# Kernel tuning notes

Hardware: AMD Instinct MI355X
Metric: run time of the kernel (lower is better)

The kernel has to match this reference:

```python
import jax, jax.numpy as jnp
import numpy as np

LEVEL_SHAPES = ((128, 128), (64, 64), (32, 32), (16, 16))  # (H_l, W_l) per level
B, LQ, C, H, L, P, DFF = 4, 1024, 256, 8, 4, 4, 1024
DH = C // H
LSRC = sum(h * w for h, w in LEVEL_SHAPES)
NORMALIZER = np.array([[w, h] for h, w in LEVEL_SHAPES], dtype=np.float32)  # (L,2) as (W,H)


def layer_norm(x, g, b, eps=1e-5):
    m = jnp.mean(x, -1, keepdims=True)
    v = jnp.var(x, -1, keepdims=True)
    return (x - m) * jax.lax.rsqrt(v + eps) * g + b


def mha(tgt, query_pos, w_in, b_in, w_out, b_out):
    # nn.MultiheadAttention with q=k=tgt+pos, v=tgt (eval mode, no dropout)
    qk = tgt + query_pos
    q = (qk @ w_in[:C].T + b_in[:C]).reshape(B, LQ, H, DH)
    k = (qk @ w_in[C:2 * C].T + b_in[C:2 * C]).reshape(B, LQ, H, DH)
    v = (tgt @ w_in[2 * C:].T + b_in[2 * C:]).reshape(B, LQ, H, DH)
    att = jax.nn.softmax(jnp.einsum('bqhd,bkhd->bhqk', q, k) / np.float32(np.sqrt(DH)), axis=-1)
    o = jnp.einsum('bhqk,bkhd->bqhd', att, v).reshape(B, LQ, C)
    return o @ w_out.T + b_out


def ms_deform_attn(query, ref, src, off_w, off_b, aw_w, aw_b, val_w, val_b, out_w, out_b):
    value = (src @ val_w.T + val_b).reshape(B, LSRC, H, DH)
    offsets = (query @ off_w.T + off_b).reshape(B, LQ, H, L, P, 2)
    aw = jax.nn.softmax((query @ aw_w.T + aw_b).reshape(B, LQ, H, L * P), axis=-1)
    aw = aw.reshape(B, LQ, H, L, P)
    # sampling locations in [0,1], offsets normalized per level by (W_l, H_l)
    loc = ref[:, :, None, :, None, :] + offsets / NORMALIZER[None, None, None, :, None, :]
    out = jnp.zeros((B, LQ, H, DH), query.dtype)
    start = 0
    for l, (h, w) in enumerate(LEVEL_SHAPES):
        v = value[:, start:start + h * w].reshape(B, h, w, H, DH)
        v = v.transpose(0, 3, 1, 2, 4).reshape(B, H, h * w, DH)  # [B,H,hw,DH]
        start += h * w
        # grid_sample semantics: align_corners=False, zero padding
        x = loc[:, :, :, l, :, 0] * w - 0.5  # [B,LQ,H,P]
        y = loc[:, :, :, l, :, 1] * h - 0.5
        x0 = jnp.floor(x); y0 = jnp.floor(y)
        x0i = x0.astype(jnp.int32); y0i = y0.astype(jnp.int32)
        wx1 = x - x0; wx0 = 1.0 - wx1
        wy1 = y - y0; wy0 = 1.0 - wy1

        def gather(ix, iy):
            valid = ((ix >= 0) & (ix < w) & (iy >= 0) & (iy < h)).astype(v.dtype)
            idx = jnp.clip(iy, 0, h - 1) * w + jnp.clip(ix, 0, w - 1)
            idx = idx.transpose(0, 2, 1, 3).reshape(B, H, LQ * P)
            g = jnp.take_along_axis(v, idx[..., None], axis=2).reshape(B, H, LQ, P, DH)
            return g * valid.transpose(0, 2, 1, 3)[..., None]

        def wmul(ww):
            return ww.transpose(0, 2, 1, 3)[..., None]  # [B,H,LQ,P,1]

        s = (gather(x0i, y0i) * wmul(wx0 * wy0)
             + gather(x0i + 1, y0i) * wmul(wx1 * wy0)
             + gather(x0i, y0i + 1) * wmul(wx0 * wy1)
             + gather(x0i + 1, y0i + 1) * wmul(wx1 * wy1))
        out = out + jnp.einsum('bhqpd,bqhp->bqhd', s, aw[:, :, :, l])
    return out.reshape(B, LQ, C) @ out_w.T + out_b


def setup_inputs():
    key = jax.random.key(0)
    ks = jax.random.split(key, 16)

    def n(i, shape, s=0.02):
        return jax.random.normal(ks[i], shape, jnp.float32) * s

    z = lambda *s: jnp.zeros(s, jnp.float32)
    o = lambda *s: jnp.ones(s, jnp.float32)
    return {
        'tgt': n(0, (B, LQ, C), 1.0),
        'query_pos': n(1, (B, LQ, C), 1.0),
        'reference_points': jax.random.uniform(ks[2], (B, LQ, L, 2), jnp.float32),
        'src': n(3, (B, LSRC, C), 1.0),
        'in_w': n(4, (3 * C, C)), 'in_b': z(3 * C),
        'sa_w': n(5, (C, C)), 'sa_b': z(C),
        'off_w': n(6, (H * L * P * 2, C)), 'off_b': n(7, (H * L * P * 2,), 2.0),
        'aw_w': n(8, (H * L * P, C)), 'aw_b': z(H * L * P),
        'val_w': n(9, (C, C)), 'val_b': z(C),
        'co_w': n(10, (C, C)), 'co_b': z(C),
        'ln1_g': o(C), 'ln1_b': z(C),
        'ln2_g': o(C), 'ln2_b': z(C),
        'ln3_g': o(C), 'ln3_b': z(C),
        'f1_w': n(11, (DFF, C)), 'f1_b': z(DFF),
        'f2_w': n(12, (C, DFF)), 'f2_b': z(C),
    }


def reference(tgt, query_pos, reference_points, src, in_w, in_b, sa_w, sa_b,
              off_w, off_b, aw_w, aw_b, val_w, val_b, co_w, co_b,
              ln1_g, ln1_b, ln2_g, ln2_b, ln3_g, ln3_b,
              f1_w, f1_b, f2_w, f2_b):
    # self-attention + residual + norm2
    tgt2 = mha(tgt, query_pos, in_w, in_b, sa_w, sa_b)
    tgt = layer_norm(tgt + tgt2, ln2_g, ln2_b)
    # multi-scale deformable cross-attention + residual + norm1 (DETR path)
    tgt2 = ms_deform_attn(tgt + query_pos, reference_points, src,
                          off_w, off_b, aw_w, aw_b, val_w, val_b, co_w, co_b)
    tgt = layer_norm(tgt + tgt2, ln1_g, ln1_b)
    # FFN + residual + norm3
    tgt2 = jax.nn.relu(tgt @ f1_w.T + f1_b) @ f2_w.T + f2_b
    tgt = layer_norm(tgt + tgt2, ln3_g, ln3_b)
    return tgt
```

## Files before the change

### kernel.cpp

```cpp
#include <hip/hip_runtime.h>
#include <hip/hip_bf16.h>
#include <math.h>

#define Bv   4
#define LQv  1024
#define Cv   256
#define Hv   8
#define Lv   4
#define Pv   4
#define DFFv 1024
#define DHv  32
#define LSRCv 21760

typedef __attribute__((ext_vector_type(8))) short bhalf8;
typedef __attribute__((ext_vector_type(4))) float floatx4;

__device__ inline unsigned pk_bf16x2(float x, float y) {
    unsigned xb = __float_as_uint(x), yb = __float_as_uint(y);
    unsigned xr = (xb + 0x7FFFu + ((xb >> 16) & 1u)) >> 16;
    unsigned yr = (yb + 0x7FFFu + ((yb >> 16) & 1u)) >> 16;
    return xr | (yr << 16);
}
__device__ inline unsigned short bf16_1(float x) {
    unsigned xb = __float_as_uint(x);
    return (unsigned short)((xb + 0x7FFFu + ((xb >> 16) & 1u)) >> 16);
}
__device__ inline float ubf2f(unsigned short u) {
    return __uint_as_float(((unsigned)u) << 16);
}

__global__ __launch_bounds__(256) void cvt_weights(const float* __restrict__ in_w,
                                                   const float* __restrict__ sa_w,
                                                   const float* __restrict__ val_w,
                                                   const float* __restrict__ off_w,
                                                   const float* __restrict__ aw_w,
                                                   const float* __restrict__ co_w,
                                                   const float* __restrict__ f1_w,
                                                   const float* __restrict__ f2_w,
                                                   const float* __restrict__ off_b,
                                                   const float* __restrict__ aw_b,
                                                   unsigned short* __restrict__ wp,
                                                   float* __restrict__ cbias) {
    const size_t idx4 = (size_t)blockIdx.x * 256 + threadIdx.x;
    if (idx4 >= 253952) {
        const int t = (int)(idx4 - 253952);
        if (t < 256) cbias[t] = off_b[t];
        else if (t < 384) cbias[t] = aw_b[t - 256];
        return;
    }
    const size_t f = idx4 * 4;
    const float* src; size_t off; int K; size_t obase; int nadd = 0;
    if (f < 196608)      { src = in_w;  off = f;          K = 256;  obase = 0; }
    else if (f < 262144) { src = sa_w;  off = f - 196608; K = 256;  obase = 196608; }
    else if (f < 327680) { src = val_w; off = f - 262144; K = 256;  obase = 262144; }
    else if (f < 393216) { src = off_w; off = f - 327680; K = 256;  obase = 327680; }
    else if (f < 425984) { src = aw_w;  off = f - 393216; K = 256;  obase = 327680; nadd = 256; }
    else if (f < 491520) { src = co_w;  off = f - 425984; K = 256;  obase = 425984; }
    else if (f < 753664) { src = f1_w;  off = f - 491520; K = 256;  obase = 491520; }
    else                 { src = f2_w;  off = f - 753664; K = 1024; obase = 753664; }
    float4 v = *(const float4*)(src + off);
    const int n = (int)(off / (size_t)K) + nadd, k = (int)(off % (size_t)K);
    const size_t di = obase + ((size_t)((n >> 4) * (K >> 5) + (k >> 5))) * 512
                    + (size_t)(((k >> 3) & 3) * 128 + (n & 15) * 8 + (k & 7));
    *(uint2*)(wp + di) = (uint2){pk_bf16x2(v.x, v.y), pk_bf16x2(v.z, v.w)};
}

__global__ __launch_bounds__(256, 4) void gemm_mfma(const float* __restrict__ A,
                                                    const float* __restrict__ A2,
                                                    const unsigned short* __restrict__ Wp,
                                                    const float* __restrict__ bias,
                                                    float* __restrict__ Cf,
                                                    unsigned short* __restrict__ Ch,
                                                    int M, int N, int K, int relu) {
    __shared__ __attribute__((aligned(16))) unsigned short As[2][64 * 136];
    const unsigned bid = blockIdx.x;
    const unsigned nc = (unsigned)N >> 6;
    const unsigned xcd = bid & 7, j = bid >> 3;
    const unsigned cpan = j % nc, r8 = j / nc;
    const int bm = (int)((xcd + (r8 << 3)) << 6);
    const int bn = (int)(cpan << 6);
    const int tid = threadIdx.x;
    const int wid = tid >> 6, lane = tid & 63;
    const int wr = wid >> 1, wc = wid & 1;
    const int col16 = lane & 15;
    const int quad = lane >> 4;

    const int srow0 = tid >> 4;
    const int scol = (tid & 15) * 4;
    const float* asrc = A + (size_t)(bm + srow0) * K + scol;
    const float* a2src = A2 ? A2 + (size_t)(bm + srow0) * K + scol : nullptr;

    const int K32 = K >> 5;
    const unsigned short* wbase = Wp + ((size_t)((bn >> 4) + wc * 2) * K32) * 512
                                + (size_t)lane * 8;

    floatx4 acc[2][2] = {};
    float4 rv[4][2];

    auto loadA = [&](int c) {
#pragma unroll
        for (int j2 = 0; j2 < 4; ++j2)
#pragma unroll
            for (int i = 0; i < 2; ++i)
                rv[j2][i] = *(const float4*)(asrc + (size_t)(16 * j2) * K + c * 128 + 64 * i);
        if (a2src) {
#pragma unroll
            for (int j2 = 0; j2 < 4; ++j2)
#pragma unroll
                for (int i = 0; i < 2; ++i) {
                    float4 t = *(const float4*)(a2src + (size_t)(16 * j2) * K + c * 128 + 64 * i);
                    rv[j2][i].x += t.x; rv[j2][i].y += t.y;
                    rv[j2][i].z += t.z; rv[j2][i].w += t.w;
                }
        }
    };
    auto writeA = [&](int buf) {
#pragma unroll
        for (int j2 = 0; j2 < 4; ++j2)
#pragma unroll
            for (int i = 0; i < 2; ++i) {
                uint2 p = {pk_bf16x2(rv[j2][i].x, rv[j2][i].y),
                           pk_bf16x2(rv[j2][i].z, rv[j2][i].w)};
                *(uint2*)&As[buf][(srow0 + 16 * j2) * 136 + scol + 64 * i] = p;
            }
    };

    const int NC = K >> 7;
    loadA(0);
    writeA(0);

    for (int c = 0; c < NC; ++c) {
        __syncthreads();
        if (c + 1 < NC) loadA(c + 1);

        const unsigned short* ab = As[c & 1];
#pragma unroll
        for (int s = 0; s < 4; ++s) {
            bhalf8 bfr[2];
#pragma unroll
            for (int nt = 0; nt < 2; ++nt)
                bfr[nt] = *(const bhalf8*)(wbase + ((size_t)(nt * K32 + c * 4 + s)) * 512);
            bhalf8 af[2];
#pragma unroll
            for (int mt = 0; mt < 2; ++mt)
                af[mt] = *(const bhalf8*)&ab[(wr * 32 + mt * 16 + col16) * 136 + s * 32 + quad * 8];
#pragma unroll
            for (int mt = 0; mt < 2; ++mt)
#pragma unroll
                for (int nt = 0; nt < 2; ++nt)
                    acc[mt][nt] = __builtin_amdgcn_mfma_f32_16x16x32_bf16(
                        af[mt], bfr[nt], acc[mt][nt], 0, 0, 0);
        }

        if (c + 1 < NC) writeA((c + 1) & 1);
    }

#pragma unroll
    for (int mt = 0; mt < 2; ++mt) {
#pragma unroll
        for (int nt = 0; nt < 2; ++nt) {
            const int col = bn + wc * 32 + nt * 16 + col16;
            const float bv = bias[col];
#pragma unroll
            for (int i = 0; i < 4; ++i) {
                const int row = bm + wr * 32 + mt * 16 + quad * 4 + i;
                float v = acc[mt][nt][i] + bv;
                if (relu) v = fmaxf(v, 0.f);
                if (Ch) Ch[(size_t)row * N + col] = bf16_1(v);
                else    Cf[(size_t)row * N + col] = v;
            }
        }
    }
}

#define ATT_SCALE 0.17677669529663687f
__global__ __launch_bounds__(256, 2) void attn_mfma(const float* __restrict__ Q,
                                                    const float* __restrict__ Kb,
                                                    const float* __restrict__ Vb,
                                                    float* __restrict__ O,
                                                    int qk_stride) {
    const int b = blockIdx.z, h = blockIdx.y, qt = blockIdx.x;
    const int tid = threadIdx.x;
    const int wid = tid >> 6, lane = tid & 63;
    const int col16 = lane & 15, quad = lane >> 4;

    __shared__ unsigned short smem_us[40960];
    unsigned short* Ks = smem_us + wid * 9600;
    unsigned short* Vt = Ks + 2560;
    unsigned short* Ps = Ks + 4864;
    float* corr_s = (float*)(Ks + 9472);
    unsigned short* Qs = smem_us + 38400;

    {
        const int row = tid >> 2, part = tid & 3;
        const float* qsrc = Q + ((size_t)(b * LQv + qt * 64 + row)) * qk_stride + h * DHv + part * 8;
        float4 qa = *(const float4*)qsrc;
        float4 qb2 = *(const float4*)(qsrc + 4);
        uint4 qp = {pk_bf16x2(qa.x * ATT_SCALE, qa.y * ATT_SCALE),
                    pk_bf16x2(qa.z * ATT_SCALE, qa.w * ATT_SCALE),
                    pk_bf16x2(qb2.x * ATT_SCALE, qb2.y * ATT_SCALE),
                    pk_bf16x2(qb2.z * ATT_SCALE, qb2.w * ATT_SCALE)};
        *(uint4*)&Qs[row * 40 + part * 8] = qp;
    }
    __syncthreads();
    bhalf8 qfr[4];
#pragma unroll
    for (int j = 0; j < 4; ++j)
        qfr[j] = *(const bhalf8*)&Qs[(j * 16 + col16) * 40 + quad * 8];

    float m_state[4] = {-1e30f, -1e30f, -1e30f, -1e30f};
    float l_state[4] = {0.f, 0.f, 0.f, 0.f};
    floatx4 acc_o[4][2] = {};
    const int dd = lane & 31, half = lane >> 5;

    const float* kbase = Kb + ((size_t)(b * LQv + wid * 256)) * qk_stride + h * DHv;
    const float* vbase = Vb + ((size_t)(b * LQv + wid * 256)) * Cv + h * DHv;

#pragma unroll 1
    for (int t = 0; t < 4; ++t) {
        {
            const float* ks = kbase + (size_t)(t * 64 + lane) * qk_stride;
            float4 f0 = *(const float4*)(ks + 0),  f1 = *(const float4*)(ks + 4);
            float4 f2 = *(const float4*)(ks + 8),  f3 = *(const float4*)(ks + 12);
            float4 f4 = *(const float4*)(ks + 16), f5 = *(const float4*)(ks + 20);
            float4 f6 = *(const float4*)(ks + 24), f7 = *(const float4*)(ks + 28);
            uint4 p0 = {pk_bf16x2(f0.x, f0.y), pk_bf16x2(f0.z, f0.w),
                        pk_bf16x2(f1.x, f1.y), pk_bf16x2(f1.z, f1.w)};
            uint4 p1 = {pk_bf16x2(f2.x, f2.y), pk_bf16x2(f2.z, f2.w),
                        pk_bf16x2(f3.x, f3.y), pk_bf16x2(f3.z, f3.w)};
            uint4 p2 = {pk_bf16x2(f4.x, f4.y), pk_bf16x2(f4.z, f4.w),
                        pk_bf16x2(f5.x, f5.y), pk_bf16x2(f5.z, f5.w)};
            uint4 p3 = {pk_bf16x2(f6.x, f6.y), pk_bf16x2(f6.z, f6.w),
                        pk_bf16x2(f7.x, f7.y), pk_bf16x2(f7.z, f7.w)};
            *(uint4*)&Ks[lane * 40 + 0]  = p0;
            *(uint4*)&Ks[lane * 40 + 8]  = p1;
            *(uint4*)&Ks[lane * 40 + 16] = p2;
            *(uint4*)&Ks[lane * 40 + 24] = p3;
        }
        {
            const float* vs = vbase + (size_t)(t * 64 + half * 32) * Cv + dd;
#pragma unroll
            for (int j4 = 0; j4 < 8; ++j4) {
                float g0 = vs[(j4 * 4 + 0) * Cv], g1 = vs[(j4 * 4 + 1) * Cv];
                float g2 = vs[(j4 * 4 + 2) * Cv], g3 = vs[(j4 * 4 + 3) * Cv];
                uint2 vp = {pk_bf16x2(g0, g1), pk_bf16x2(g2, g3)};
                *(uint2*)&Vt[dd * 72 + half * 32 + j4 * 4] = vp;
            }
        }

        floatx4 accs[4][4] = {};
        bhalf8 af[4];
#pragma unroll
        for (int kf = 0; kf < 4; ++kf)
            af[kf] = *(const bhalf8*)&Ks[(kf * 16 + col16) * 40 + quad * 8];
#pragma unroll
        for (int kf = 0; kf < 4; ++kf)
#pragma unroll
            for (int qf = 0; qf < 4; ++qf)
                accs[kf][qf] = __builtin_amdgcn_mfma_f32_16x16x32_bf16(
                    af[kf], qfr[qf], accs[kf][qf], 0, 0, 0);

#pragma unroll
        for (int qf = 0; qf < 4; ++qf) {
            float tmax = -1e30f;
#pragma unroll
            for (int kf = 0; kf < 4; ++kf) {
                tmax = fmaxf(tmax, fmaxf(fmaxf(accs[kf][qf][0], accs[kf][qf][1]),
                                         fmaxf(accs[kf][qf][2], accs[kf][qf][3])));
            }
            tmax = fmaxf(tmax, __shfl_xor(tmax, 16));
            tmax = fmaxf(tmax, __shfl_xor(tmax, 32));
            float mnew = fmaxf(m_state[qf], tmax);
            float cr = __expf(m_state[qf] - mnew);
            m_state[qf] = mnew;
            float psum = 0.f;
#pragma unroll
            for (int kf = 0; kf < 4; ++kf) {
                float p0 = __expf(accs[kf][qf][0] - mnew);
                float p1 = __expf(accs[kf][qf][1] - mnew);
                float p2 = __expf(accs[kf][qf][2] - mnew);
                float p3 = __expf(accs[kf][qf][3] - mnew);
                psum += (p0 + p1) + (p2 + p3);
                uint2 pp = {pk_bf16x2(p0, p1), pk_bf16x2(p2, p3)};
                *(uint2*)&Ps[(qf * 16 + col16) * 72 + kf * 16 + quad * 4] = pp;
            }
            psum += __shfl_xor(psum, 16);
            psum += __shfl_xor(psum, 32);
            l_state[qf] = l_state[qf] * cr + psum;
            if (quad == 0) corr_s[qf * 16 + col16] = cr;
        }

#pragma unroll
        for (int mf = 0; mf < 4; ++mf) {
            float4 cv = *(const float4*)&corr_s[mf * 16 + quad * 4];
#pragma unroll
            for (int nf = 0; nf < 2; ++nf) {
                acc_o[mf][nf][0] *= cv.x;
                acc_o[mf][nf][1] *= cv.y;
                acc_o[mf][nf][2] *= cv.z;
                acc_o[mf][nf][3] *= cv.w;
            }
        }
#pragma unroll
        for (int ks2 = 0; ks2 < 2; ++ks2) {
            bhalf8 pf[4], vf[2];
#pragma unroll
            for (int mf = 0; mf < 4; ++mf)
                pf[mf] = *(const bhalf8*)&Ps[(mf * 16 + col16) * 72 + ks2 * 32 + quad * 8];
#pragma unroll
            for (int nf = 0; nf < 2; ++nf)
                vf[nf] = *(const bhalf8*)&Vt[(nf * 16 + col16) * 72 + ks2 * 32 + quad * 8];
#pragma unroll
            for (int mf = 0; mf < 4; ++mf)
#pragma unroll
                for (int nf = 0; nf < 2; ++nf)
                    acc_o[mf][nf] = __builtin_amdgcn_mfma_f32_16x16x32_bf16(
                        pf[mf], vf[nf], acc_o[mf][nf], 0, 0, 0);
        }
    }

    __syncthreads();
    float* mbuf = (float*)smem_us;
    float* lbuf = mbuf + 256;
    float* obuf = lbuf + 256;
    if (quad == 0) {
#pragma unroll
        for (int qf = 0; qf < 4; ++qf) {
            mbuf[wid * 64 + qf * 16 + col16] = m_state[qf];
            lbuf[wid * 64 + qf * 16 + col16] = l_state[qf];
        }
    }
#pragma unroll
    for (int mf = 0; mf < 4; ++mf)
#pragma unroll
        for (int nf = 0; nf < 2; ++nf)
#pragma unroll
            for (int i = 0; i < 4; ++i)
                obuf[wid * 2048 + (mf * 16 + quad * 4 + i) * 32 + nf * 16 + col16] =
                    acc_o[mf][nf][i];
    __syncthreads();
    {
        const int q = tid >> 2, dg = (tid & 3) * 8;
        float m0 = mbuf[q], m1 = mbuf[64 + q], m2 = mbuf[128 + q], m3 = mbuf[192 + q];
        float gm = fmaxf(fmaxf(m0, m1), fmaxf(m2, m3));
        float e0 = __expf(m0 - gm), e1 = __expf(m1 - gm);
        float e2 = __expf(m2 - gm), e3 = __expf(m3 - gm);
        float lt = lbuf[q] * e0 + lbuf[64 + q] * e1 + lbuf[128 + q] * e2 + lbuf[192 + q] * e3;
        float inv = 1.f / lt;
        const float* o0 = obuf + q * 32 + dg;
        float* orow = O + ((size_t)(b * LQv + qt * 64 + q)) * Cv + h * DHv + dg;
        float ov[8];
#pragma unroll
        for (int d = 0; d < 8; ++d)
            ov[d] = (o0[d] * e0 + o0[2048 + d] * e1 + o0[4096 + d] * e2 + o0[6144 + d] * e3) * inv;
        *(float4*)(orow) = make_float4(ov[0], ov[1], ov[2], ov[3]);
        *(float4*)(orow + 4) = make_float4(ov[4], ov[5], ov[6], ov[7]);
    }
}

__global__ __launch_bounds__(256) void deform_sample(const unsigned short* __restrict__ value,
                                                     const float* __restrict__ oab,
                                                     const float* __restrict__ ref,
                                                     float* __restrict__ out) {
    const int bq = blockIdx.x;
    const int b = bq >> 10;
    const int tid = threadIdx.x;
    const int h = tid >> 5, d = tid & 31;

    const float* aw = oab + (size_t)bq * 384 + 256 + h * 16;
    float w[16];
    float mx = -1e30f;
#pragma unroll
    for (int j = 0; j < 16; ++j) { w[j] = aw[j]; mx = fmaxf(mx, w[j]); }
    float ssum = 0.f;
#pragma unroll
    for (int j = 0; j < 16; ++j) { w[j] = __expf(w[j] - mx); ssum += w[j]; }
    float invs = 1.f / ssum;

    const float* op = oab + (size_t)bq * 384 + h * 32;
    const float* rp = ref + (size_t)bq * (Lv * 2);

    const int starts[4] = {0, 16384, 20480, 21504};
    const int WHl[4] = {128, 64, 32, 16};

    float acc = 0.f;
#pragma unroll 1
    for (int l = 0; l < 4; ++l) {
        const int wl = WHl[l];
        const float rx = rp[l * 2 + 0], ry = rp[l * 2 + 1];
        const unsigned short* vb0 = value + ((size_t)b * LSRCv + starts[l]) * Cv + h * DHv + d;
#pragma unroll 1
        for (int p = 0; p < 4; ++p) {
            float ox = op[l * 8 + p * 2 + 0], oy = op[l * 8 + p * 2 + 1];
            float x = rx * (float)wl + ox - 0.5f;
            float y = ry * (float)wl + oy - 0.5f;
            float fx0 = floorf(x), fy0 = floorf(y);
            int x0 = (int)fx0, y0 = (int)fy0;
            float tx = x - fx0, ty = y - fy0;
            float w00 = (1.f - tx) * (1.f - ty);
            float w10 = tx * (1.f - ty);
            float w01 = (1.f - tx) * ty;
            float w11 = tx * ty;
            float s = 0.f;
            bool xin0 = (x0 >= 0) & (x0 < wl);
            bool xin1 = (x0 + 1 >= 0) & (x0 + 1 < wl);
            bool yin0 = (y0 >= 0) & (y0 < wl);
            bool yin1 = (y0 + 1 >= 0) & (y0 + 1 < wl);
            if (yin0) {
                if (xin0) s = fmaf(w00, ubf2f(vb0[(size_t)(y0 * wl + x0) * Cv]), s);
                if (xin1) s = fmaf(w10, ubf2f(vb0[(size_t)(y0 * wl + x0 + 1) * Cv]), s);
            }
            if (yin1) {
                if (xin0) s = fmaf(w01, ubf2f(vb0[(size_t)((y0 + 1) * wl + x0) * Cv]), s);
                if (xin1) s = fmaf(w11, ubf2f(vb0[(size_t)((y0 + 1) * wl + x0 + 1) * Cv]), s);
            }
            acc = fmaf(w[l * 4 + p] * invs, s, acc);
        }
    }
    out[(size_t)bq * Cv + h * DHv + d] = acc;
}

__global__ __launch_bounds__(256) void ln_residual(const float* __restrict__ x,
                                                   const float* __restrict__ r,
                                                   const float* __restrict__ g,
                                                   const float* __restrict__ bta,
                                                   float* __restrict__ out) {
    const int row = blockIdx.x;
    const int tid = threadIdx.x;
    float v = x[(size_t)row * Cv + tid] + r[(size_t)row * Cv + tid];
    float s = v, sq = v * v;
#pragma unroll
    for (int off = 32; off > 0; off >>= 1) {
        s  += __shfl_down(s, off, 64);
        sq += __shfl_down(sq, off, 64);
    }
    __shared__ float ss[4], sqq[4];
    int wid = tid >> 6;
    if ((tid & 63) == 0) { ss[wid] = s; sqq[wid] = sq; }
    __syncthreads();
    __shared__ float meansh, rstdsh;
    if (tid == 0) {
        float S = ss[0] + ss[1] + ss[2] + ss[3];
        float Q = sqq[0] + sqq[1] + sqq[2] + sqq[3];
        float mean = S * (1.f / Cv);
        float var = Q * (1.f / Cv) - mean * mean;
        meansh = mean;
        rstdsh = rsqrtf(var + 1e-5f);
    }
    __syncthreads();
    out[(size_t)row * Cv + tid] = (v - meansh) * rstdsh * g[tid] + bta[tid];
}

extern "C" void kernel_launch(void* const* d_in, const int* in_sizes, int n_in,
                              void* d_out, int out_size, void* d_ws, size_t ws_size,
                              hipStream_t stream) {
    const float* tgt       = (const float*)d_in[0];
    const float* query_pos = (const float*)d_in[1];
    const float* ref_pts   = (const float*)d_in[2];
    const float* src       = (const float*)d_in[3];
    const float* in_w      = (const float*)d_in[4];
    const float* in_b      = (const float*)d_in[5];
    const float* sa_w      = (const float*)d_in[6];
    const float* sa_b      = (const float*)d_in[7];
    const float* off_w     = (const float*)d_in[8];
    const float* off_b     = (const float*)d_in[9];
    const float* aw_w      = (const float*)d_in[10];
    const float* aw_b      = (const float*)d_in[11];
    const float* val_w     = (const float*)d_in[12];
    const float* val_b     = (const float*)d_in[13];
    const float* co_w      = (const float*)d_in[14];
    const float* co_b      = (const float*)d_in[15];
    const float* ln1_g     = (const float*)d_in[16];
    const float* ln1_b     = (const float*)d_in[17];
    const float* ln2_g     = (const float*)d_in[18];
    const float* ln2_b     = (const float*)d_in[19];
    const float* ln3_g     = (const float*)d_in[20];
    const float* ln3_b     = (const float*)d_in[21];
    const float* f1_w      = (const float*)d_in[22];
    const float* f1_b      = (const float*)d_in[23];
    const float* f2_w      = (const float*)d_in[24];
    const float* f2_b      = (const float*)d_in[25];

    const int M0  = Bv * LQv * Cv;
    const int VSZ = Bv * LSRCv * Cv;
    float* ws = (float*)d_ws;

    float* big    = ws;
    float* qkbuf  = big;
    float* vb     = big + (size_t)2 * M0;
    float* ob     = big + (size_t)3 * M0;
    unsigned short* value16 = (unsigned short*)big;
    unsigned short* wb = (unsigned short*)(big + (size_t)20000000);
    float* cbias  = big + (size_t)20510000;
    float* tgt_a  = ws + (size_t)VSZ;
    float* oabuf  = tgt_a + M0;
    float* sampled= oabuf + (size_t)Bv * LQv * 384;
    float* tgt_b  = sampled + M0;
    float* hidden = tgt_b + M0;
    float* tmp    = hidden + (size_t)Bv * LQv * DFFv;

    const size_t WB_IN = 0, WB_SA = 196608, WB_VAL = 262144, WB_OA = 327680,
                 WB_CO = 425984, WB_F1 = 491520, WB_F2 = 753664;

    const int Mq = Bv * LQv;
    dim3 blk256(256);

    cvt_weights<<<dim3(993), blk256, 0, stream>>>(
        in_w, sa_w, val_w, off_w, aw_w, co_w, f1_w, f2_w, off_b, aw_b, wb, cbias);

    gemm_mfma<<<dim3((Mq / 64) * (512 / 64)), blk256, 0, stream>>>(
        tgt, query_pos, wb + WB_IN, in_b, qkbuf, nullptr, Mq, 512, Cv, 0);
    gemm_mfma<<<dim3((Mq / 64) * (Cv / 64)), blk256, 0, stream>>>(
        tgt, nullptr, wb + WB_IN + 131072, in_b + 2 * Cv, vb, nullptr, Mq, Cv, Cv, 0);

    attn_mfma<<<dim3(LQv / 64, Hv, Bv), blk256, 0, stream>>>(qkbuf, qkbuf + 256, vb, ob, 512);

    gemm_mfma<<<dim3((Mq / 64) * (Cv / 64)), blk256, 0, stream>>>(
        ob, nullptr, wb + WB_SA, sa_b, tmp, nullptr, Mq, Cv, Cv, 0);
    ln_residual<<<dim3(Mq), blk256, 0, stream>>>(tgt, tmp, ln2_g, ln2_b, tgt_a);

    gemm_mfma<<<dim3(((Bv * LSRCv) / 64) * (Cv / 64)), blk256, 0, stream>>>(
        src, nullptr, wb + WB_VAL, val_b, nullptr, value16, Bv * LSRCv, Cv, Cv, 0);

    gemm_mfma<<<dim3((Mq / 64) * (384 / 64)), blk256, 0, stream>>>(
        tgt_a, query_pos, wb + WB_OA, cbias, oabuf, nullptr, Mq, 384, Cv, 0);

    deform_sample<<<dim3(Bv * LQv), blk256, 0, stream>>>(value16, oabuf, ref_pts, sampled);

    gemm_mfma<<<dim3((Mq / 64) * (Cv / 64)), blk256, 0, stream>>>(
        sampled, nullptr, wb + WB_CO, co_b, tmp, nullptr, Mq, Cv, Cv, 0);
    ln_residual<<<dim3(Mq), blk256, 0, stream>>>(tgt_a, tmp, ln1_g, ln1_b, tgt_b);

    gemm_mfma<<<dim3((Mq / 64) * (DFFv / 64)), blk256, 0, stream>>>(
        tgt_b, nullptr, wb + WB_F1, f1_b, hidden, nullptr, Mq, DFFv, Cv, 1);
    gemm_mfma<<<dim3((Mq / 64) * (Cv / 64)), blk256, 0, stream>>>(
        hidden, nullptr, wb + WB_F2, f2_b, tmp, nullptr, Mq, Cv, DFFv, 0);
    ln_residual<<<dim3(Mq), blk256, 0, stream>>>(tgt_b, tmp, ln3_g, ln3_b, (float*)d_out);
}
```

Measured before the change: 371.5 us.

## Keep GEMM weight fragments in registers and loop over multiple row panels per block

For K=256 GEMMs, each block now loads its full 64-column weight slice into registers once and reuses it across NP row panels. The value projection launches one fifth as many blocks, each covering 5 panels, with A loads pipelined through double-buffered shared memory. The aim is to cut repeated weight fetches and block launch overhead on the large value GEMM. In exchange it raises register pressure (launch bounds drop from 4 to 3) and reduces grid parallelism. Bias loads are also hoisted.

```diff
diff --git a/kernel.cpp b/kernel.cpp
--- a/kernel.cpp
+++ b/kernel.cpp
@@ -65,19 +65,21 @@
     *(uint2*)(wp + di) = (uint2){pk_bf16x2(v.x, v.y), pk_bf16x2(v.z, v.w)};
 }
 
-__global__ __launch_bounds__(256, 4) void gemm_mfma(const float* __restrict__ A,
+__global__ __launch_bounds__(256, 3) void gemm_mfma(const float* __restrict__ A,
                                                     const float* __restrict__ A2,
                                                     const unsigned short* __restrict__ Wp,
                                                     const float* __restrict__ bias,
                                                     float* __restrict__ Cf,
                                                     unsigned short* __restrict__ Ch,
-                                                    int M, int N, int K, int relu) {
+                                                    int M, int N, int K, int relu,
+                                                    int NP) {
     __shared__ __attribute__((aligned(16))) unsigned short As[2][64 * 136];
     const unsigned bid = blockIdx.x;
     const unsigned nc = (unsigned)N >> 6;
     const unsigned xcd = bid & 7, j = bid >> 3;
-    const unsigned cpan = j % nc, r8 = j / nc;
-    const int bm = (int)((xcd + (r8 << 3)) << 6);
+    const unsigned cpan = j % nc, gk = j / nc;
+    const int grp = (int)(xcd + 8 * gk);
+    const int bm0 = grp * NP * 64;
     const int bn = (int)(cpan << 6);
     const int tid = threadIdx.x;
     const int wid = tid >> 6, lane = tid & 63;
@@ -87,28 +89,34 @@
 
     const int srow0 = tid >> 4;
     const int scol = (tid & 15) * 4;
-    const float* asrc = A + (size_t)(bm + srow0) * K + scol;
-    const float* a2src = A2 ? A2 + (size_t)(bm + srow0) * K + scol : nullptr;
+    const float* asrc = A + (size_t)(bm0 + srow0) * K + scol;
+    const float* a2src = A2 ? A2 + (size_t)(bm0 + srow0) * K + scol : nullptr;
 
     const int K32 = K >> 5;
     const unsigned short* wbase = Wp + ((size_t)((bn >> 4) + wc * 2) * K32) * 512
                                 + (size_t)lane * 8;
 
+    float bv[2];
+    bv[0] = bias[bn + wc * 32 + col16];
+    bv[1] = bias[bn + wc * 32 + 16 + col16];
+
     floatx4 acc[2][2] = {};
     float4 rv[4][2];
 
-    auto loadA = [&](int c) {
+    auto loadA = [&](int p, int c) {
+        const float* base = asrc + (size_t)(p * 64) * K + c * 128;
 #pragma unroll
         for (int j2 = 0; j2 < 4; ++j2)
 #pragma unroll
             for (int i = 0; i < 2; ++i)
-                rv[j2][i] = *(const float4*)(asrc + (size_t)(16 * j2) * K + c * 128 + 64 * i);
+                rv[j2][i] = *(const float4*)(base + (size_t)(16 * j2) * K + 64 * i);
         if (a2src) {
+            const float* base2 = a2src + (size_t)(p * 64) * K + c * 128;
 #pragma unroll
             for (int j2 = 0; j2 < 4; ++j2)
 #pragma unroll
                 for (int i = 0; i < 2; ++i) {
-                    float4 t = *(const float4*)(a2src + (size_t)(16 * j2) * K + c * 128 + 64 * i);
+                    float4 t = *(const float4*)(base2 + (size_t)(16 * j2) * K + 64 * i);
                     rv[j2][i].x += t.x; rv[j2][i].y += t.y;
                     rv[j2][i].z += t.z; rv[j2][i].w += t.w;
                 }
@@ -125,51 +133,116 @@
             }
     };
 
-    const int NC = K >> 7;
-    loadA(0);
-    writeA(0);
-
-    for (int c = 0; c < NC; ++c) {
-        __syncthreads();
-        if (c + 1 < NC) loadA(c + 1);
-
-        const unsigned short* ab = As[c & 1];
-#pragma unroll
-        for (int s = 0; s < 4; ++s) {
-            bhalf8 bfr[2];
+    if (K32 == 8) {
+        bhalf8 wfr[2][8];
+#pragma unroll
+        for (int nt = 0; nt < 2; ++nt)
+#pragma unroll
+            for (int k2 = 0; k2 < 8; ++k2)
+                wfr[nt][k2] = *(const bhalf8*)(wbase + (size_t)(nt * 8 + k2) * 512);
+
+        loadA(0, 0);
+        writeA(0);
+
+        for (int p = 0; p < NP; ++p) {
+            __syncthreads();
+            loadA(p, 1);
+            {
+                const unsigned short* ab = As[0];
+#pragma unroll
+                for (int s = 0; s < 4; ++s) {
+                    bhalf8 af[2];
+#pragma unroll
+                    for (int mt = 0; mt < 2; ++mt)
+                        af[mt] = *(const bhalf8*)&ab[(wr * 32 + mt * 16 + col16) * 136 + s * 32 + quad * 8];
+#pragma unroll
+                    for (int mt = 0; mt < 2; ++mt)
+#pragma unroll
+                        for (int nt = 0; nt < 2; ++nt)
+                            acc[mt][nt] = __builtin_amdgcn_mfma_f32_16x16x32_bf16(
+                                af[mt], wfr[nt][s], acc[mt][nt], 0, 0, 0);
+                }
+            }
+            writeA(1);
+
+            __syncthreads();
+            if (p + 1 < NP) loadA(p + 1, 0);
+            {
+                const unsigned short* ab = As[1];
+#pragma unroll
+                for (int s = 0; s < 4; ++s) {
+                    bhalf8 af[2];
+#pragma unroll
+                    for (int mt = 0; mt < 2; ++mt)
+                        af[mt] = *(const bhalf8*)&ab[(wr * 32 + mt * 16 + col16) * 136 + s * 32 + quad * 8];
+#pragma unroll
+                    for (int mt = 0; mt < 2; ++mt)
+#pragma unroll
+                        for (int nt = 0; nt < 2; ++nt)
+                            acc[mt][nt] = __builtin_amdgcn_mfma_f32_16x16x32_bf16(
+                                af[mt], wfr[nt][4 + s], acc[mt][nt], 0, 0, 0);
+                }
+            }
+
+            {
+                const int rowb = bm0 + p * 64 + wr * 32;
+#pragma unroll
+                for (int mt = 0; mt < 2; ++mt)
+#pragma unroll
+                    for (int nt = 0; nt < 2; ++nt)
+#pragma unroll
+                        for (int i = 0; i < 4; ++i) {
+                            const int col = bn + wc * 32 + nt * 16 + col16;
+                            const int row = rowb + mt * 16 + quad * 4 + i;
+                            float v = acc[mt][nt][i] + bv[nt];
+                            if (relu) v = fmaxf(v, 0.f);
+                            if (Ch) Ch[(size_t)row * N + col] = bf16_1(v);
+                            else    Cf[(size_t)row * N + col] = v;
+                            acc[mt][nt][i] = 0.f;
+                        }
+            }
+            if (p + 1 < NP) writeA(0);
+        }
+    } else {
+        const int NC = K >> 7;
+        loadA(0, 0);
+        writeA(0);
+        for (int c = 0; c < NC; ++c) {
+            __syncthreads();
+            if (c + 1 < NC) loadA(0, c + 1);
+            const unsigned short* ab = As[c & 1];
+#pragma unroll
+            for (int s = 0; s < 4; ++s) {
+                bhalf8 bfr[2];
+#pragma unroll
+                for (int nt = 0; nt < 2; ++nt)
+                    bfr[nt] = *(const bhalf8*)(wbase + ((size_t)(nt * K32 + c * 4 + s)) * 512);
+                bhalf8 af[2];
+#pragma unroll
+                for (int mt = 0; mt < 2; ++mt)
+                    af[mt] = *(const bhalf8*)&ab[(wr * 32 + mt * 16 + col16) * 136 + s * 32 + quad * 8];
+#pragma unroll
+                for (int mt = 0; mt < 2; ++mt)
+#pragma unroll
+                    for (int nt = 0; nt < 2; ++nt)
+                        acc[mt][nt] = __builtin_amdgcn_mfma_f32_16x16x32_bf16(
+                            af[mt], bfr[nt], acc[mt][nt], 0, 0, 0);
+            }
+            if (c + 1 < NC) writeA((c + 1) & 1);
+        }
+#pragma unroll
+        for (int mt = 0; mt < 2; ++mt)
 #pragma unroll
             for (int nt = 0; nt < 2; ++nt)
-                bfr[nt] = *(const bhalf8*)(wbase + ((size_t)(nt * K32 + c * 4 + s)) * 512);
-            bhalf8 af[2];
-#pragma unroll
-            for (int mt = 0; mt < 2; ++mt)
-                af[mt] = *(const bhalf8*)&ab[(wr * 32 + mt * 16 + col16) * 136 + s * 32 + quad * 8];
-#pragma unroll
-            for (int mt = 0; mt < 2; ++mt)
-#pragma unroll
-                for (int nt = 0; nt < 2; ++nt)
-                    acc[mt][nt] = __builtin_amdgcn_mfma_f32_16x16x32_bf16(
-                        af[mt], bfr[nt], acc[mt][nt], 0, 0, 0);
-        }
-
-        if (c + 1 < NC) writeA((c + 1) & 1);
-    }
-
-#pragma unroll
-    for (int mt = 0; mt < 2; ++mt) {
-#pragma unroll
-        for (int nt = 0; nt < 2; ++nt) {
-            const int col = bn + wc * 32 + nt * 16 + col16;
-            const float bv = bias[col];
-#pragma unroll
-            for (int i = 0; i < 4; ++i) {
-                const int row = bm + wr * 32 + mt * 16 + quad * 4 + i;
-                float v = acc[mt][nt][i] + bv;
-                if (relu) v = fmaxf(v, 0.f);
-                if (Ch) Ch[(size_t)row * N + col] = bf16_1(v);
-                else    Cf[(size_t)row * N + col] = v;
-            }
-        }
+#pragma unroll
+                for (int i = 0; i < 4; ++i) {
+                    const int col = bn + wc * 32 + nt * 16 + col16;
+                    const int row = bm0 + wr * 32 + mt * 16 + quad * 4 + i;
+                    float v = acc[mt][nt][i] + bv[nt];
+                    if (relu) v = fmaxf(v, 0.f);
+                    if (Ch) Ch[(size_t)row * N + col] = bf16_1(v);
+                    else    Cf[(size_t)row * N + col] = v;
+                }
     }
 }
 
@@ -509,31 +582,31 @@
         in_w, sa_w, val_w, off_w, aw_w, co_w, f1_w, f2_w, off_b, aw_b, wb, cbias);
 
     gemm_mfma<<<dim3((Mq / 64) * (512 / 64)), blk256, 0, stream>>>(
-        tgt, query_pos, wb + WB_IN, in_b, qkbuf, nullptr, Mq, 512, Cv, 0);
+        tgt, query_pos, wb + WB_IN, in_b, qkbuf, nullptr, Mq, 512, Cv, 0, 1);
     gemm_mfma<<<dim3((Mq / 64) * (Cv / 64)), blk256, 0, stream>>>(
-        tgt, nullptr, wb + WB_IN + 131072, in_b + 2 * Cv, vb, nullptr, Mq, Cv, Cv, 0);
+        tgt, nullptr, wb + WB_IN + 131072, in_b + 2 * Cv, vb, nullptr, Mq, Cv, Cv, 0, 1);
 
     attn_mfma<<<dim3(LQv / 64, Hv, Bv), blk256, 0, stream>>>(qkbuf, qkbuf + 256, vb, ob, 512);
 
     gemm_mfma<<<dim3((Mq / 64) * (Cv / 64)), blk256, 0, stream>>>(
-        ob, nullptr, wb + WB_SA, sa_b, tmp, nullptr, Mq, Cv, Cv, 0);
+        ob, nullptr, wb + WB_SA, sa_b, tmp, nullptr, Mq, Cv, Cv, 0, 1);
     ln_residual<<<dim3(Mq), blk256, 0, stream>>>(tgt, tmp, ln2_g, ln2_b, tgt_a);
 
-    gemm_mfma<<<dim3(((Bv * LSRCv) / 64) * (Cv / 64)), blk256, 0, stream>>>(
-        src, nullptr, wb + WB_VAL, val_b, nullptr, value16, Bv * LSRCv, Cv, Cv, 0);
+    gemm_mfma<<<dim3((((Bv * LSRCv) / 64) / 5) * (Cv / 64)), blk256, 0, stream>>>(
+        src, nullptr, wb + WB_VAL, val_b, nullptr, value16, Bv * LSRCv, Cv, Cv, 0, 5);
 
     gemm_mfma<<<dim3((Mq / 64) * (384 / 64)), blk256, 0, stream>>>(
-        tgt_a, query_pos, wb + WB_OA, cbias, oabuf, nullptr, Mq, 384, Cv, 0);
+        tgt_a, query_pos, wb + WB_OA, cbias, oabuf, nullptr, Mq, 384, Cv, 0, 1);
 
     deform_sample<<<dim3(Bv * LQv), blk256, 0, stream>>>(value16, oabuf, ref_pts, sampled);
 
     gemm_mfma<<<dim3((Mq / 64) * (Cv / 64)), blk256, 0, stream>>>(
-        sampled, nullptr, wb + WB_CO, co_b, tmp, nullptr, Mq, Cv, Cv, 0);
+        sampled, nullptr, wb + WB_CO, co_b, tmp, nullptr, Mq, Cv, Cv, 0, 1);
     ln_residual<<<dim3(Mq), blk256, 0, stream>>>(tgt_a, tmp, ln1_g, ln1_b, tgt_b);
 
     gemm_mfma<<<dim3((Mq / 64) * (DFFv / 64)), blk256, 0, stream>>>(
-        tgt_b, nullptr, wb + WB_F1, f1_b, hidden, nullptr, Mq, DFFv, Cv, 1);
+        tgt_b, nullptr, wb + WB_F1, f1_b, hidden, nullptr, Mq, DFFv, Cv, 1, 1);
     gemm_mfma<<<dim3((Mq / 64) * (Cv / 64)), blk256, 0, stream>>>(
-        hidden, nullptr, wb + WB_F2, f2_b, tmp, nullptr, Mq, Cv, DFFv, 0);
+        hidden, nullptr, wb + WB_F2, f2_b, tmp, nullptr, Mq, Cv, DFFv, 0, 1);
     ln_residual<<<dim3(Mq), blk256, 0, stream>>>(tgt_b, tmp, ln3_g, ln3_b, (float*)d_out);
 }
```

New measurement: 383.4 us. +3.2%, slower.
